# Performance work log

Measured on AMD Instinct MI355X. Metric: run time of the kernel, lower is better.

## Reference

```python
import jax, jax.numpy as jnp
import numpy as np

B, T, M, C, H = 2, 2048, 2048, 1024, 16
D = C // H  # head_size = 64


def setup_inputs() -> dict:
    key = jax.random.key(0)
    ks = jax.random.split(key, 8)
    s = 0.02
    return {
        "relative_positions": jax.random.normal(ks[0], (H, T, T + M), jnp.float32),
        "x": jax.random.normal(ks[1], (B, T, C), jnp.float32),
        "xl_memory": jax.random.normal(ks[2], (B, M, 2, C), jnp.float32),
        "Wq": jax.random.normal(ks[3], (C, C), jnp.float32) * s,
        "Wk": jax.random.normal(ks[4], (C, C), jnp.float32) * s,
        "Wv": jax.random.normal(ks[5], (C, C), jnp.float32) * s,
        "Wp": jax.random.normal(ks[6], (C, C), jnp.float32) * s,
        "bp": jax.random.normal(ks[7], (C,), jnp.float32) * s,
    }


def reference(relative_positions, x, xl_memory, Wq, Wk, Wv, Wp, bp):
    b, t, c = x.shape
    h, d = H, D
    q = x @ Wq  # [b,t,c]
    k = x @ Wk
    v = x @ Wv
    k_xl = xl_memory[..., 0, :]  # [b,m,c]
    v_xl = xl_memory[..., 1, :]
    k = jnp.concatenate([k_xl, k], axis=-2)  # [b,t+m,c]
    v = jnp.concatenate([v_xl, v], axis=-2)
    tk = k.shape[1]

    def split_heads(z):  # [b,s,(h d)] -> [b,h,s,d]
        return z.reshape(z.shape[0], z.shape[1], h, d).transpose(0, 2, 1, 3)

    qh, kh, vh = split_heads(q), split_heads(k), split_heads(v)
    w = jnp.einsum("bhid,bhjd->bhij", qh, kh)  # [b,h,t,tk]
    i, j = w.shape[-2], w.shape[-1]
    # bias added BEFORE scaling, as in the original
    w = (w + relative_positions[..., -i:, -j:]) * (d ** -0.5)
    # causal mask with memory offset: mask where col > row + (j - i)
    row = jnp.arange(i)[:, None]
    col = jnp.arange(j)[None, :]
    mask = col > row + (j - i)
    w = jnp.where(mask, -jnp.inf, w)
    w = jax.nn.softmax(w, axis=-1)
    wv = jnp.einsum("bhij,bhjd->bhid", w, vh)  # [b,h,t,d]
    wv = wv.transpose(0, 2, 1, 3).reshape(b, t, c)
    out = wv @ Wp + bp
    # rebuild xl memory from full-length k,v, keep last T steps
    k_flat = kh.transpose(0, 2, 1, 3).reshape(b, tk, c)
    v_flat = vh.transpose(0, 2, 1, 3).reshape(b, tk, c)
    new_xl_memory = jnp.stack([k_flat, v_flat], axis=-2)[:, -t:]  # [b,t,2,c]
    return out, new_xl_memory
```

## Files before the change

### kernel.cpp

```cpp
#include <hip/hip_runtime.h>
#include <hip/hip_bf16.h>

constexpr int NB  = 2;
constexpr int TT  = 2048;
constexpr int MEM = 2048;
constexpr int CC  = 1024;
constexpr int NH  = 16;
constexpr int HD  = 64;
constexpr int TKK = 4096;
constexpr int BT  = NB * TT;

typedef __attribute__((ext_vector_type(8))) short short8;
typedef __attribute__((ext_vector_type(4))) float floatx4;

struct __align__(8) us4 { unsigned short x, y, z, w; };

__device__ __forceinline__ unsigned short f2bf(float f) {
  union { float f; unsigned int u; } v; v.f = f;
  return (unsigned short)((v.u + 0x7fffu + ((v.u >> 16) & 1u)) >> 16);
}

__global__ __launch_bounds__(256) void prep_xl_k(const float* __restrict__ xl,
    unsigned short* __restrict__ k_ws, unsigned short* __restrict__ v_ws) {
  int idx = blockIdx.x * 256 + threadIdx.x;
  int c   = (idx & 255) << 2;
  int rem = idx >> 8;
  int m   = rem & 2047;
  int b   = rem >> 11;
  size_t src = ((size_t)(b * MEM + m)) * 2 * CC + c;
  float4 kk = *(const float4*)&xl[src];
  float4 vv = *(const float4*)&xl[src + CC];
  int h = c >> 6, d = c & 63;
  size_t dst = ((size_t)((b * NH + h) * TKK) + m) * HD + d;
  *(us4*)&k_ws[dst] = us4{f2bf(kk.x), f2bf(kk.y), f2bf(kk.z), f2bf(kk.w)};
  *(us4*)&v_ws[dst] = us4{f2bf(vv.x), f2bf(vv.y), f2bf(vv.z), f2bf(vv.w)};
}

__global__ __launch_bounds__(256) void gemm_qkv_k(
    const float* __restrict__ x, const float* __restrict__ Wq,
    const float* __restrict__ Wk, const float* __restrict__ Wv,
    unsigned short* __restrict__ q_ws, unsigned short* __restrict__ k_ws,
    unsigned short* __restrict__ v_ws, float* __restrict__ out_xl) {
  __shared__ unsigned short As[128][32];
  __shared__ unsigned short Bs[128][40];
  const int tid = threadIdx.x;
  const int m0 = blockIdx.x * 128;
  const int nb = blockIdx.y;
  const float* __restrict__ Wsrc = (nb < 8) ? Wq : ((nb < 16) ? Wk : Wv);
  const int n0 = (nb & 7) * 128;
  const int wave = tid >> 6, lane = tid & 63;
  const int mh = (wave >> 1) * 64, nh = (wave & 1) * 64;
  const int ln = lane & 15, qd = lane >> 4;
  const floatx4 fzero = {0.f, 0.f, 0.f, 0.f};

  floatx4 acc[4][4];
#pragma unroll
  for (int i = 0; i < 4; i++)
#pragma unroll
    for (int j = 0; j < 4; j++) acc[i][j] = fzero;

  for (int kt = 0; kt < CC; kt += 32) {
    __syncthreads();
#pragma unroll
    for (int i = 0; i < 4; i++) {
      int e = tid + i * 256;
      int row = e >> 3, kc = (e & 7) << 2;
      float4 a4 = *(const float4*)&x[(size_t)(m0 + row) * CC + kt + kc];
      *(us4*)&As[row][kc] = us4{f2bf(a4.x), f2bf(a4.y), f2bf(a4.z), f2bf(a4.w)};
    }
#pragma unroll
    for (int i = 0; i < 4; i++) {
      int e = tid + i * 256;
      int n = e & 127, kg = e >> 7;
      const float* p = &Wsrc[(size_t)(kt + kg * 4) * CC + n0 + n];
      float b0 = p[0], b1 = p[CC], b2 = p[2 * CC], b3 = p[3 * CC];
      *(us4*)&Bs[n][kg * 4] = us4{f2bf(b0), f2bf(b1), f2bf(b2), f2bf(b3)};
    }
    __syncthreads();
    short8 af[4], bfr[4];
#pragma unroll
    for (int mf = 0; mf < 4; mf++) af[mf]  = *(const short8*)&As[mh + mf * 16 + ln][qd * 8];
#pragma unroll
    for (int nf = 0; nf < 4; nf++) bfr[nf] = *(const short8*)&Bs[nh + nf * 16 + ln][qd * 8];
#pragma unroll
    for (int mf = 0; mf < 4; mf++)
#pragma unroll
      for (int nf = 0; nf < 4; nf++)
        acc[mf][nf] = __builtin_amdgcn_mfma_f32_16x16x32_bf16(af[mf], bfr[nf], acc[mf][nf], 0, 0, 0);
  }

  const int sel = nb >> 3;
#pragma unroll
  for (int mf = 0; mf < 4; mf++) {
#pragma unroll
    for (int nf = 0; nf < 4; nf++) {
      int gn = n0 + nh + nf * 16 + ln;
      int h = gn >> 6, d = gn & 63;
#pragma unroll
      for (int r = 0; r < 4; r++) {
        int gm = m0 + mh + mf * 16 + qd * 4 + r;
        int b = gm >> 11, t = gm & 2047;
        float val = acc[mf][nf][r];
        unsigned short bv = f2bf(val);
        if (sel == 0) {
          q_ws[((size_t)((b * NH + h) * TT) + t) * HD + d] = bv;
        } else if (sel == 1) {
          k_ws[((size_t)((b * NH + h) * TKK) + MEM + t) * HD + d] = bv;
          out_xl[(((size_t)(b * TT + t)) * 2 + 0) * CC + gn] = val;
        } else {
          v_ws[((size_t)((b * NH + h) * TKK) + MEM + t) * HD + d] = bv;
          out_xl[(((size_t)(b * TT + t)) * 2 + 1) * CC + gn] = val;
        }
      }
    }
  }
}

__global__ __launch_bounds__(256) void attn_k(
    const unsigned short* __restrict__ q_ws, const unsigned short* __restrict__ k_ws,
    const unsigned short* __restrict__ v_ws, const float* __restrict__ rel,
    unsigned short* __restrict__ wv_ws) {
  __shared__ unsigned short Ks[NB][64][72];
  __shared__ unsigned short Vs[NB][64][64];
  __shared__ unsigned short Ps[4][16][64];
  const int qt = blockIdx.x, h = blockIdx.y;
  const int tid = threadIdx.x;
  const int wave = tid >> 6, lane = tid & 63;
  const int ln = lane & 15, qd = lane >> 4;
  const int q0 = qt * 64;
  const int qrow_w = q0 + wave * 16;
  const floatx4 fzero = {0.f, 0.f, 0.f, 0.f};

  short8 qf[NB][2];
#pragma unroll
  for (int b = 0; b < NB; b++)
#pragma unroll
    for (int ks = 0; ks < 2; ks++)
      qf[b][ks] = *(const short8*)&q_ws[((size_t)((b * NH + h) * TT) + qrow_w + ln) * HD + ks * 32 + qd * 8];

  floatx4 of[NB][4];
  float mrow[NB][4], lrow[NB][4];
#pragma unroll
  for (int b = 0; b < NB; b++) {
#pragma unroll
    for (int nf = 0; nf < 4; nf++) of[b][nf] = fzero;
#pragma unroll
    for (int r = 0; r < 4; r++) { mrow[b][r] = -1e30f; lrow[b][r] = 0.f; }
  }

  const int ntiles = qt + 33;
  for (int kt = 0; kt < ntiles; kt++) {
    const int kbase = kt * 64;
    __syncthreads();
#pragma unroll
    for (int b = 0; b < NB; b++) {
      const size_t rowbase = (size_t)((b * NH + h) * TKK) + kbase;
#pragma unroll
      for (int i = 0; i < 2; i++) {
        int e = tid + i * 256;
        int r = e >> 3, c0 = (e & 7) << 3;
        *(short8*)&Ks[b][r][c0] = *(const short8*)&k_ws[(rowbase + r) * HD + c0];
        short8 v8 = *(const short8*)&v_ws[(rowbase + r) * HD + c0];
#pragma unroll
        for (int j = 0; j < 8; j++) {
          int d = c0 + j;
          int slot = ((r >> 3) ^ (d & 7) ^ (d >> 3)) & 7;
          Vs[b][d][(slot << 3) | (r & 7)] = (unsigned short)v8[j];
        }
      }
    }
    __syncthreads();

    float bias[4][4];
#pragma unroll
    for (int nf = 0; nf < 4; nf++)
#pragma unroll
      for (int r = 0; r < 4; r++)
        bias[nf][r] = rel[((size_t)(h * TT) + qrow_w + qd * 4 + r) * TKK + kbase + nf * 16 + ln];

    const bool lastTile = (kt == ntiles - 1);

#pragma unroll
    for (int b = 0; b < NB; b++) {
      floatx4 sacc[4];
#pragma unroll
      for (int nf = 0; nf < 4; nf++) sacc[nf] = fzero;
#pragma unroll
      for (int ks = 0; ks < 2; ks++)
#pragma unroll
        for (int nf = 0; nf < 4; nf++) {
          short8 kf = *(const short8*)&Ks[b][nf * 16 + ln][ks * 32 + qd * 8];
          sacc[nf] = __builtin_amdgcn_mfma_f32_16x16x32_bf16(qf[b][ks], kf, sacc[nf], 0, 0, 0);
        }

      float sv[4][4];
#pragma unroll
      for (int nf = 0; nf < 4; nf++)
#pragma unroll
        for (int r = 0; r < 4; r++)
          sv[nf][r] = (sacc[nf][r] + bias[nf][r]) * 0.125f;
      if (lastTile) {
#pragma unroll
        for (int nf = 0; nf < 4; nf++)
#pragma unroll
          for (int r = 0; r < 4; r++) {
            int kcol = kbase + nf * 16 + ln;
            int qrow = qrow_w + qd * 4 + r;
            if (kcol > qrow + MEM) sv[nf][r] = -1e30f;
          }
      }

#pragma unroll
      for (int r = 0; r < 4; r++) {
        float mx = fmaxf(fmaxf(sv[0][r], sv[1][r]), fmaxf(sv[2][r], sv[3][r]));
#pragma unroll
        for (int off = 8; off >= 1; off >>= 1)
          mx = fmaxf(mx, __shfl_xor(mx, off, 64));
        float mnew = fmaxf(mrow[b][r], mx);
        float alpha = __expf(mrow[b][r] - mnew);
        mrow[b][r] = mnew;
        float sum = 0.f;
#pragma unroll
        for (int nf = 0; nf < 4; nf++) {
          float p = __expf(sv[nf][r] - mnew);
          sv[nf][r] = p;
          sum += p;
        }
#pragma unroll
        for (int off = 8; off >= 1; off >>= 1)
          sum += __shfl_xor(sum, off, 64);
        lrow[b][r] = lrow[b][r] * alpha + sum;
#pragma unroll
        for (int nf = 0; nf < 4; nf++) of[b][nf][r] *= alpha;
      }

#pragma unroll
      for (int nf = 0; nf < 4; nf++)
#pragma unroll
        for (int r = 0; r < 4; r++) {
          int row = qd * 4 + r;
          int col = nf * 16 + ln;
          int slot = ((col >> 3) ^ (row & 7) ^ (row >> 3)) & 7;
          Ps[wave][row][(slot << 3) | (col & 7)] = f2bf(sv[nf][r]);
        }

#pragma unroll
      for (int ks = 0; ks < 2; ks++) {
        int g = qd + 4 * ks;
        int pslot = (g ^ (ln & 7) ^ (ln >> 3)) & 7;
        short8 pf = *(const short8*)&Ps[wave][ln][pslot << 3];
#pragma unroll
        for (int nf = 0; nf < 4; nf++) {
          int dd = nf * 16 + ln;
          int vslot = (g ^ (dd & 7) ^ (dd >> 3)) & 7;
          short8 vf = *(const short8*)&Vs[b][dd][vslot << 3];
          of[b][nf] = __builtin_amdgcn_mfma_f32_16x16x32_bf16(pf, vf, of[b][nf], 0, 0, 0);
        }
      }
    }
  }

#pragma unroll
  for (int b = 0; b < NB; b++) {
    float inv[4];
#pragma unroll
    for (int r = 0; r < 4; r++) inv[r] = 1.f / lrow[b][r];
#pragma unroll
    for (int nf = 0; nf < 4; nf++)
#pragma unroll
      for (int r = 0; r < 4; r++)
        wv_ws[((size_t)(b * TT) + qrow_w + qd * 4 + r) * CC + h * 64 + nf * 16 + ln] =
            f2bf(of[b][nf][r] * inv[r]);
  }
}

__global__ __launch_bounds__(256) void gemm_out_k(
    const unsigned short* __restrict__ a_bf, const float* __restrict__ Wp,
    const float* __restrict__ bp, float* __restrict__ out) {
  __shared__ unsigned short As[128][32];
  __shared__ unsigned short Bs[128][40];
  const int tid = threadIdx.x;
  const int m0 = blockIdx.x * 128;
  const int n0 = blockIdx.y * 128;
  const int wave = tid >> 6, lane = tid & 63;
  const int mh = (wave >> 1) * 64, nh = (wave & 1) * 64;
  const int ln = lane & 15, qd = lane >> 4;
  const floatx4 fzero = {0.f, 0.f, 0.f, 0.f};

  floatx4 acc[4][4];
#pragma unroll
  for (int i = 0; i < 4; i++)
#pragma unroll
    for (int j = 0; j < 4; j++) acc[i][j] = fzero;

  for (int kt = 0; kt < CC; kt += 32) {
    __syncthreads();
#pragma unroll
    for (int i = 0; i < 2; i++) {
      int e = tid + i * 256;
      int row = e >> 2, c0 = (e & 3) << 3;
      *(short8*)&As[row][c0] = *(const short8*)&a_bf[(size_t)(m0 + row) * CC + kt + c0];
    }
#pragma unroll
    for (int i = 0; i < 4; i++) {
      int e = tid + i * 256;
      int n = e & 127, kg = e >> 7;
      const float* p = &Wp[(size_t)(kt + kg * 4) * CC + n0 + n];
      float b0 = p[0], b1 = p[CC], b2 = p[2 * CC], b3 = p[3 * CC];
      *(us4*)&Bs[n][kg * 4] = us4{f2bf(b0), f2bf(b1), f2bf(b2), f2bf(b3)};
    }
    __syncthreads();
    short8 af[4], bfr[4];
#pragma unroll
    for (int mf = 0; mf < 4; mf++) af[mf]  = *(const short8*)&As[mh + mf * 16 + ln][qd * 8];
#pragma unroll
    for (int nf = 0; nf < 4; nf++) bfr[nf] = *(const short8*)&Bs[nh + nf * 16 + ln][qd * 8];
#pragma unroll
    for (int mf = 0; mf < 4; mf++)
#pragma unroll
      for (int nf = 0; nf < 4; nf++)
        acc[mf][nf] = __builtin_amdgcn_mfma_f32_16x16x32_bf16(af[mf], bfr[nf], acc[mf][nf], 0, 0, 0);
  }

#pragma unroll
  for (int mf = 0; mf < 4; mf++)
#pragma unroll
    for (int nf = 0; nf < 4; nf++) {
      int gn = n0 + nh + nf * 16 + ln;
      float bias = bp[gn];
#pragma unroll
      for (int r = 0; r < 4; r++) {
        int gm = m0 + mh + mf * 16 + qd * 4 + r;
        out[(size_t)gm * CC + gn] = acc[mf][nf][r] + bias;
      }
    }
}

extern "C" void kernel_launch(void* const* d_in, const int* in_sizes, int n_in,
                              void* d_out, int out_size, void* d_ws, size_t ws_size,
                              hipStream_t stream) {
  const float* rel = (const float*)d_in[0];
  const float* x   = (const float*)d_in[1];
  const float* xl  = (const float*)d_in[2];
  const float* Wq  = (const float*)d_in[3];
  const float* Wk  = (const float*)d_in[4];
  const float* Wv  = (const float*)d_in[5];
  const float* Wp  = (const float*)d_in[6];
  const float* bp  = (const float*)d_in[7];
  float* out    = (float*)d_out;
  float* out_xl = out + (size_t)BT * CC;

  char* ws = (char*)d_ws;
  unsigned short* q_ws  = (unsigned short*)(ws);
  unsigned short* k_ws  = (unsigned short*)(ws + (size_t)(8)  * 1024 * 1024);
  unsigned short* v_ws  = (unsigned short*)(ws + (size_t)(24) * 1024 * 1024);
  unsigned short* wv_ws = (unsigned short*)(ws + (size_t)(40) * 1024 * 1024);

  prep_xl_k<<<dim3(4096), dim3(256), 0, stream>>>(xl, k_ws, v_ws);
  gemm_qkv_k<<<dim3(32, 24), dim3(256), 0, stream>>>(x, Wq, Wk, Wv, q_ws, k_ws, v_ws, out_xl);
  attn_k<<<dim3(32, 16), dim3(256), 0, stream>>>(q_ws, k_ws, v_ws, rel, wv_ws);
  gemm_out_k<<<dim3(32, 8), dim3(256), 0, stream>>>(wv_ws, Wp, bp, out);
}
```

Before: 1.043 ms.

## Pre-transpose weights, pre-swizzle V, split attention per batch with register prefetch

Adds a kernel that converts Wq/Wk/Wv to bf16 and transposes them once, so the QKV GEMM loads B tiles with vector reads instead of strided scalar float reads. V is stored in a pre-swizzled transposed tile layout, so attention copies it straight into LDS without a per-element scatter. Attention now launches one block per (batch, query tile), which doubles the grid. It prefetches the next K/V tile into registers and computes the softmax denominator with an MFMA against a ones vector instead of shuffle reductions. The extra kernels and the Wt/wv_ws workspace aliasing (both at offset 40MB, used at different times) add launches and some risk, and the denominator is now summed from bf16-rounded probabilities.

```diff
diff --git a/kernel.cpp b/kernel.cpp
--- a/kernel.cpp
+++ b/kernel.cpp
@@ -19,35 +19,79 @@
   union { float f; unsigned int u; } v; v.f = f;
   return (unsigned short)((v.u + 0x7fffu + ((v.u >> 16) & 1u)) >> 16);
 }
+__device__ __forceinline__ unsigned short f2bf_fast(float f) {
+  union { float f; unsigned int u; } v; v.f = f;
+  return (unsigned short)((v.u + 0x8000u) >> 16);
+}
+
+__global__ __launch_bounds__(256) void prep_w_k(
+    const float* __restrict__ Wq, const float* __restrict__ Wk,
+    const float* __restrict__ Wv, unsigned short* __restrict__ Wt) {
+  __shared__ unsigned short T[64][72];
+  const int n0 = blockIdx.x * 64, k0 = blockIdx.y * 64, z = blockIdx.z;
+  const float* __restrict__ W = (z == 0) ? Wq : ((z == 1) ? Wk : Wv);
+  const int tid = threadIdx.x;
+#pragma unroll
+  for (int s = 0; s < 4; s++) {
+    int kr = (tid >> 4) + s * 16, nc = (tid & 15) << 2;
+    float4 w4 = *(const float4*)&W[(size_t)(k0 + kr) * CC + n0 + nc];
+    T[nc + 0][kr] = f2bf(w4.x);
+    T[nc + 1][kr] = f2bf(w4.y);
+    T[nc + 2][kr] = f2bf(w4.z);
+    T[nc + 3][kr] = f2bf(w4.w);
+  }
+  __syncthreads();
+#pragma unroll
+  for (int i = 0; i < 2; i++) {
+    int e = tid + i * 256;
+    int n = e >> 3, kc = (e & 7) << 3;
+    *(short8*)&Wt[(size_t)z * CC * CC + (size_t)(n0 + n) * CC + k0 + kc] =
+        *(const short8*)&T[n][kc];
+  }
+}
 
 __global__ __launch_bounds__(256) void prep_xl_k(const float* __restrict__ xl,
     unsigned short* __restrict__ k_ws, unsigned short* __restrict__ v_ws) {
-  int idx = blockIdx.x * 256 + threadIdx.x;
-  int c   = (idx & 255) << 2;
-  int rem = idx >> 8;
-  int m   = rem & 2047;
-  int b   = rem >> 11;
-  size_t src = ((size_t)(b * MEM + m)) * 2 * CC + c;
-  float4 kk = *(const float4*)&xl[src];
-  float4 vv = *(const float4*)&xl[src + CC];
-  int h = c >> 6, d = c & 63;
-  size_t dst = ((size_t)((b * NH + h) * TKK) + m) * HD + d;
-  *(us4*)&k_ws[dst] = us4{f2bf(kk.x), f2bf(kk.y), f2bf(kk.z), f2bf(kk.w)};
-  *(us4*)&v_ws[dst] = us4{f2bf(vv.x), f2bf(vv.y), f2bf(vv.z), f2bf(vv.w)};
+  __shared__ unsigned short T[64][72];
+  const int mt = blockIdx.x, h = blockIdx.y, b = blockIdx.z;
+  const int tid = threadIdx.x;
+  const int bh = b * NH + h;
+#pragma unroll
+  for (int s = 0; s < 4; s++) {
+    int m = (tid >> 4) + s * 16, d4 = (tid & 15) << 2;
+    size_t src = ((size_t)(b * MEM + mt * 64 + m)) * 2 * CC + h * 64 + d4;
+    float4 kk = *(const float4*)&xl[src];
+    float4 vv = *(const float4*)&xl[src + CC];
+    *(us4*)&k_ws[((size_t)bh * TKK + mt * 64 + m) * HD + d4] =
+        us4{f2bf(kk.x), f2bf(kk.y), f2bf(kk.z), f2bf(kk.w)};
+    T[d4 + 0][m] = f2bf(vv.x);
+    T[d4 + 1][m] = f2bf(vv.y);
+    T[d4 + 2][m] = f2bf(vv.z);
+    T[d4 + 3][m] = f2bf(vv.w);
+  }
+  __syncthreads();
+  const size_t vbase = ((size_t)bh * 64 + mt) * 4096;
+#pragma unroll
+  for (int i = 0; i < 2; i++) {
+    int e = tid + i * 256;
+    int d = e >> 3, mc = (e & 7) << 3;
+    int grp = (mc >> 3) ^ (d & 7);
+    *(short8*)&v_ws[vbase + d * 64 + (grp << 3)] = *(const short8*)&T[d][mc];
+  }
 }
 
 __global__ __launch_bounds__(256) void gemm_qkv_k(
-    const float* __restrict__ x, const float* __restrict__ Wq,
-    const float* __restrict__ Wk, const float* __restrict__ Wv,
+    const float* __restrict__ x, const unsigned short* __restrict__ Wt,
     unsigned short* __restrict__ q_ws, unsigned short* __restrict__ k_ws,
     unsigned short* __restrict__ v_ws, float* __restrict__ out_xl) {
-  __shared__ unsigned short As[128][32];
+  __shared__ unsigned short As[128][40];
   __shared__ unsigned short Bs[128][40];
   const int tid = threadIdx.x;
   const int m0 = blockIdx.x * 128;
   const int nb = blockIdx.y;
-  const float* __restrict__ Wsrc = (nb < 8) ? Wq : ((nb < 16) ? Wk : Wv);
+  const int sel = nb >> 3;
   const int n0 = (nb & 7) * 128;
+  const unsigned short* __restrict__ Wsel = Wt + (size_t)sel * CC * CC;
   const int wave = tid >> 6, lane = tid & 63;
   const int mh = (wave >> 1) * 64, nh = (wave & 1) * 64;
   const int ln = lane & 15, qd = lane >> 4;
@@ -69,12 +113,10 @@
       *(us4*)&As[row][kc] = us4{f2bf(a4.x), f2bf(a4.y), f2bf(a4.z), f2bf(a4.w)};
     }
 #pragma unroll
-    for (int i = 0; i < 4; i++) {
+    for (int i = 0; i < 2; i++) {
       int e = tid + i * 256;
-      int n = e & 127, kg = e >> 7;
-      const float* p = &Wsrc[(size_t)(kt + kg * 4) * CC + n0 + n];
-      float b0 = p[0], b1 = p[CC], b2 = p[2 * CC], b3 = p[3 * CC];
-      *(us4*)&Bs[n][kg * 4] = us4{f2bf(b0), f2bf(b1), f2bf(b2), f2bf(b3)};
+      int n = e >> 2, kc = (e & 3) << 3;
+      *(short8*)&Bs[n][kc] = *(const short8*)&Wsel[(size_t)(n0 + n) * CC + kt + kc];
     }
     __syncthreads();
     short8 af[4], bfr[4];
@@ -89,7 +131,6 @@
         acc[mf][nf] = __builtin_amdgcn_mfma_f32_16x16x32_bf16(af[mf], bfr[nf], acc[mf][nf], 0, 0, 0);
   }
 
-  const int sel = nb >> 3;
 #pragma unroll
   for (int mf = 0; mf < 4; mf++) {
 #pragma unroll
@@ -100,15 +141,19 @@
       for (int r = 0; r < 4; r++) {
         int gm = m0 + mh + mf * 16 + qd * 4 + r;
         int b = gm >> 11, t = gm & 2047;
+        int bh = b * NH + h;
         float val = acc[mf][nf][r];
         unsigned short bv = f2bf(val);
         if (sel == 0) {
-          q_ws[((size_t)((b * NH + h) * TT) + t) * HD + d] = bv;
+          q_ws[((size_t)bh * TT + t) * HD + d] = bv;
         } else if (sel == 1) {
-          k_ws[((size_t)((b * NH + h) * TKK) + MEM + t) * HD + d] = bv;
+          k_ws[((size_t)bh * TKK + MEM + t) * HD + d] = bv;
           out_xl[(((size_t)(b * TT + t)) * 2 + 0) * CC + gn] = val;
         } else {
-          v_ws[((size_t)((b * NH + h) * TKK) + MEM + t) * HD + d] = bv;
+          int kk = MEM + t;
+          int kblk = kk >> 6;
+          int grp = ((t >> 3) & 7) ^ (d & 7);
+          v_ws[((size_t)bh * 64 + kblk) * 4096 + d * 64 + (grp << 3) + (t & 7)] = bv;
           out_xl[(((size_t)(b * TT + t)) * 2 + 1) * CC + gn] = val;
         }
       }
@@ -116,168 +161,170 @@
   }
 }
 
-__global__ __launch_bounds__(256) void attn_k(
+__global__ __launch_bounds__(256, 4) void attn_k(
     const unsigned short* __restrict__ q_ws, const unsigned short* __restrict__ k_ws,
     const unsigned short* __restrict__ v_ws, const float* __restrict__ rel,
     unsigned short* __restrict__ wv_ws) {
-  __shared__ unsigned short Ks[NB][64][72];
-  __shared__ unsigned short Vs[NB][64][64];
+  __shared__ unsigned short Ks[64][72];
+  __shared__ unsigned short Vs[64 * 64];
   __shared__ unsigned short Ps[4][16][64];
-  const int qt = blockIdx.x, h = blockIdx.y;
+  const int bx = blockIdx.x;
+  const int b = bx & 1, qt = bx >> 1;
+  const int h = blockIdx.y;
   const int tid = threadIdx.x;
   const int wave = tid >> 6, lane = tid & 63;
   const int ln = lane & 15, qd = lane >> 4;
   const int q0 = qt * 64;
   const int qrow_w = q0 + wave * 16;
+  const int bh = b * NH + h;
   const floatx4 fzero = {0.f, 0.f, 0.f, 0.f};
 
-  short8 qf[NB][2];
-#pragma unroll
-  for (int b = 0; b < NB; b++)
-#pragma unroll
-    for (int ks = 0; ks < 2; ks++)
-      qf[b][ks] = *(const short8*)&q_ws[((size_t)((b * NH + h) * TT) + qrow_w + ln) * HD + ks * 32 + qd * 8];
-
-  floatx4 of[NB][4];
-  float mrow[NB][4], lrow[NB][4];
-#pragma unroll
-  for (int b = 0; b < NB; b++) {
-#pragma unroll
-    for (int nf = 0; nf < 4; nf++) of[b][nf] = fzero;
-#pragma unroll
-    for (int r = 0; r < 4; r++) { mrow[b][r] = -1e30f; lrow[b][r] = 0.f; }
-  }
+  const unsigned short* __restrict__ kbaseP = k_ws + (size_t)bh * TKK * HD;
+  const unsigned short* __restrict__ vbaseP = v_ws + (size_t)bh * 64 * 4096;
+  const float* __restrict__ relBase = rel + ((size_t)h * TT + qrow_w + qd * 4) * TKK + ln;
+
+  short8 qf[2];
+#pragma unroll
+  for (int ks = 0; ks < 2; ks++)
+    qf[ks] = *(const short8*)&q_ws[((size_t)bh * TT + qrow_w + ln) * HD + ks * 32 + qd * 8];
+
+  short8 ones;
+#pragma unroll
+  for (int j = 0; j < 8; j++) ones[j] = (short)0x3F80;
+
+  floatx4 of[4], osum = fzero;
+  float mrow[4];
+#pragma unroll
+  for (int nf = 0; nf < 4; nf++) of[nf] = fzero;
+#pragma unroll
+  for (int r = 0; r < 4; r++) mrow[r] = -1e30f;
 
   const int ntiles = qt + 33;
+  short8 kpre0, kpre1, vpre0, vpre1;
+  {
+    const unsigned short* kp = kbaseP;
+    const unsigned short* vp = vbaseP;
+    kpre0 = *(const short8*)(kp + tid * 8);
+    kpre1 = *(const short8*)(kp + tid * 8 + 2048);
+    vpre0 = *(const short8*)(vp + tid * 8);
+    vpre1 = *(const short8*)(vp + tid * 8 + 2048);
+  }
+
   for (int kt = 0; kt < ntiles; kt++) {
     const int kbase = kt * 64;
     __syncthreads();
-#pragma unroll
-    for (int b = 0; b < NB; b++) {
-      const size_t rowbase = (size_t)((b * NH + h) * TKK) + kbase;
-#pragma unroll
-      for (int i = 0; i < 2; i++) {
-        int e = tid + i * 256;
-        int r = e >> 3, c0 = (e & 7) << 3;
-        *(short8*)&Ks[b][r][c0] = *(const short8*)&k_ws[(rowbase + r) * HD + c0];
-        short8 v8 = *(const short8*)&v_ws[(rowbase + r) * HD + c0];
-#pragma unroll
-        for (int j = 0; j < 8; j++) {
-          int d = c0 + j;
-          int slot = ((r >> 3) ^ (d & 7) ^ (d >> 3)) & 7;
-          Vs[b][d][(slot << 3) | (r & 7)] = (unsigned short)v8[j];
+    {
+      int r0 = tid >> 3, c0 = (tid & 7) << 3;
+      *(short8*)&Ks[r0][c0] = kpre0;
+      *(short8*)&Ks[r0 + 32][c0] = kpre1;
+      *(short8*)&Vs[tid * 8] = vpre0;
+      *(short8*)&Vs[tid * 8 + 2048] = vpre1;
+    }
+    __syncthreads();
+    if (kt + 1 < ntiles) {
+      const unsigned short* kp = kbaseP + (kt + 1) * 4096;
+      const unsigned short* vp = vbaseP + (kt + 1) * 4096;
+      kpre0 = *(const short8*)(kp + tid * 8);
+      kpre1 = *(const short8*)(kp + tid * 8 + 2048);
+      vpre0 = *(const short8*)(vp + tid * 8);
+      vpre1 = *(const short8*)(vp + tid * 8 + 2048);
+    }
+
+    float bias[4][4];
+#pragma unroll
+    for (int nf = 0; nf < 4; nf++)
+#pragma unroll
+      for (int r = 0; r < 4; r++)
+        bias[nf][r] = relBase[(size_t)r * TKK + kbase + nf * 16];
+
+    floatx4 sacc[4];
+#pragma unroll
+    for (int nf = 0; nf < 4; nf++) sacc[nf] = fzero;
+#pragma unroll
+    for (int ks = 0; ks < 2; ks++)
+#pragma unroll
+      for (int nf = 0; nf < 4; nf++) {
+        short8 kf = *(const short8*)&Ks[nf * 16 + ln][ks * 32 + qd * 8];
+        sacc[nf] = __builtin_amdgcn_mfma_f32_16x16x32_bf16(qf[ks], kf, sacc[nf], 0, 0, 0);
+      }
+
+    float sv[4][4];
+#pragma unroll
+    for (int nf = 0; nf < 4; nf++)
+#pragma unroll
+      for (int r = 0; r < 4; r++)
+        sv[nf][r] = (sacc[nf][r] + bias[nf][r]) * 0.125f;
+
+    if (kt == ntiles - 1) {
+#pragma unroll
+      for (int nf = 0; nf < 4; nf++)
+#pragma unroll
+        for (int r = 0; r < 4; r++) {
+          int kcol = kbase + nf * 16 + ln;
+          int qrow = qrow_w + qd * 4 + r;
+          if (kcol > qrow + MEM) sv[nf][r] = -1e30f;
         }
-      }
-    }
-    __syncthreads();
-
-    float bias[4][4];
+    }
+
+#pragma unroll
+    for (int r = 0; r < 4; r++) {
+      float mx = fmaxf(fmaxf(sv[0][r], sv[1][r]), fmaxf(sv[2][r], sv[3][r]));
+#pragma unroll
+      for (int off = 8; off >= 1; off >>= 1)
+        mx = fmaxf(mx, __shfl_xor(mx, off, 64));
+      float mnew = fmaxf(mrow[r], mx);
+      float alpha = __expf(mrow[r] - mnew);
+      mrow[r] = mnew;
+#pragma unroll
+      for (int nf = 0; nf < 4; nf++) {
+        float p = __expf(sv[nf][r] - mnew);
+        sv[nf][r] = p;
+        of[nf][r] *= alpha;
+      }
+      osum[r] *= alpha;
+    }
+
 #pragma unroll
     for (int nf = 0; nf < 4; nf++)
 #pragma unroll
-      for (int r = 0; r < 4; r++)
-        bias[nf][r] = rel[((size_t)(h * TT) + qrow_w + qd * 4 + r) * TKK + kbase + nf * 16 + ln];
-
-    const bool lastTile = (kt == ntiles - 1);
-
-#pragma unroll
-    for (int b = 0; b < NB; b++) {
-      floatx4 sacc[4];
-#pragma unroll
-      for (int nf = 0; nf < 4; nf++) sacc[nf] = fzero;
-#pragma unroll
-      for (int ks = 0; ks < 2; ks++)
-#pragma unroll
-        for (int nf = 0; nf < 4; nf++) {
-          short8 kf = *(const short8*)&Ks[b][nf * 16 + ln][ks * 32 + qd * 8];
-          sacc[nf] = __builtin_amdgcn_mfma_f32_16x16x32_bf16(qf[b][ks], kf, sacc[nf], 0, 0, 0);
-        }
-
-      float sv[4][4];
-#pragma unroll
-      for (int nf = 0; nf < 4; nf++)
-#pragma unroll
-        for (int r = 0; r < 4; r++)
-          sv[nf][r] = (sacc[nf][r] + bias[nf][r]) * 0.125f;
-      if (lastTile) {
-#pragma unroll
-        for (int nf = 0; nf < 4; nf++)
-#pragma unroll
-          for (int r = 0; r < 4; r++) {
-            int kcol = kbase + nf * 16 + ln;
-            int qrow = qrow_w + qd * 4 + r;
-            if (kcol > qrow + MEM) sv[nf][r] = -1e30f;
-          }
-      }
-
-#pragma unroll
       for (int r = 0; r < 4; r++) {
-        float mx = fmaxf(fmaxf(sv[0][r], sv[1][r]), fmaxf(sv[2][r], sv[3][r]));
-#pragma unroll
-        for (int off = 8; off >= 1; off >>= 1)
-          mx = fmaxf(mx, __shfl_xor(mx, off, 64));
-        float mnew = fmaxf(mrow[b][r], mx);
-        float alpha = __expf(mrow[b][r] - mnew);
-        mrow[b][r] = mnew;
-        float sum = 0.f;
-#pragma unroll
-        for (int nf = 0; nf < 4; nf++) {
-          float p = __expf(sv[nf][r] - mnew);
-          sv[nf][r] = p;
-          sum += p;
-        }
-#pragma unroll
-        for (int off = 8; off >= 1; off >>= 1)
-          sum += __shfl_xor(sum, off, 64);
-        lrow[b][r] = lrow[b][r] * alpha + sum;
-#pragma unroll
-        for (int nf = 0; nf < 4; nf++) of[b][nf][r] *= alpha;
-      }
-
-#pragma unroll
-      for (int nf = 0; nf < 4; nf++)
-#pragma unroll
-        for (int r = 0; r < 4; r++) {
-          int row = qd * 4 + r;
-          int col = nf * 16 + ln;
-          int slot = ((col >> 3) ^ (row & 7) ^ (row >> 3)) & 7;
-          Ps[wave][row][(slot << 3) | (col & 7)] = f2bf(sv[nf][r]);
-        }
-
-#pragma unroll
-      for (int ks = 0; ks < 2; ks++) {
-        int g = qd + 4 * ks;
-        int pslot = (g ^ (ln & 7) ^ (ln >> 3)) & 7;
-        short8 pf = *(const short8*)&Ps[wave][ln][pslot << 3];
-#pragma unroll
-        for (int nf = 0; nf < 4; nf++) {
-          int dd = nf * 16 + ln;
-          int vslot = (g ^ (dd & 7) ^ (dd >> 3)) & 7;
-          short8 vf = *(const short8*)&Vs[b][dd][vslot << 3];
-          of[b][nf] = __builtin_amdgcn_mfma_f32_16x16x32_bf16(pf, vf, of[b][nf], 0, 0, 0);
-        }
-      }
-    }
-  }
-
-#pragma unroll
-  for (int b = 0; b < NB; b++) {
-    float inv[4];
-#pragma unroll
-    for (int r = 0; r < 4; r++) inv[r] = 1.f / lrow[b][r];
-#pragma unroll
-    for (int nf = 0; nf < 4; nf++)
-#pragma unroll
-      for (int r = 0; r < 4; r++)
-        wv_ws[((size_t)(b * TT) + qrow_w + qd * 4 + r) * CC + h * 64 + nf * 16 + ln] =
-            f2bf(of[b][nf][r] * inv[r]);
-  }
+        int row = qd * 4 + r;
+        int col = nf * 16 + ln;
+        int slot = ((col >> 3) ^ (row & 7) ^ (row >> 3)) & 7;
+        Ps[wave][row][(slot << 3) | (col & 7)] = f2bf_fast(sv[nf][r]);
+      }
+
+#pragma unroll
+    for (int ks = 0; ks < 2; ks++) {
+      int g = ks * 4 + qd;
+      int pslot = (g ^ (ln & 7) ^ (ln >> 3)) & 7;
+      short8 pf = *(const short8*)&Ps[wave][ln][pslot << 3];
+      osum = __builtin_amdgcn_mfma_f32_16x16x32_bf16(pf, ones, osum, 0, 0, 0);
+#pragma unroll
+      for (int nf = 0; nf < 4; nf++) {
+        int dd = nf * 16 + ln;
+        int vgrp = g ^ (dd & 7);
+        short8 vf = *(const short8*)&Vs[dd * 64 + (vgrp << 3)];
+        of[nf] = __builtin_amdgcn_mfma_f32_16x16x32_bf16(pf, vf, of[nf], 0, 0, 0);
+      }
+    }
+  }
+
+  float inv[4];
+#pragma unroll
+  for (int r = 0; r < 4; r++) inv[r] = 1.f / osum[r];
+#pragma unroll
+  for (int nf = 0; nf < 4; nf++)
+#pragma unroll
+    for (int r = 0; r < 4; r++)
+      wv_ws[((size_t)(b * TT) + qrow_w + qd * 4 + r) * CC + h * 64 + nf * 16 + ln] =
+          f2bf(of[nf][r] * inv[r]);
 }
 
 __global__ __launch_bounds__(256) void gemm_out_k(
     const unsigned short* __restrict__ a_bf, const float* __restrict__ Wp,
     const float* __restrict__ bp, float* __restrict__ out) {
-  __shared__ unsigned short As[128][32];
+  __shared__ unsigned short As[128][40];
   __shared__ unsigned short Bs[128][40];
   const int tid = threadIdx.x;
   const int m0 = blockIdx.x * 128;
@@ -352,12 +399,14 @@
 
   char* ws = (char*)d_ws;
   unsigned short* q_ws  = (unsigned short*)(ws);
-  unsigned short* k_ws  = (unsigned short*)(ws + (size_t)(8)  * 1024 * 1024);
-  unsigned short* v_ws  = (unsigned short*)(ws + (size_t)(24) * 1024 * 1024);
-  unsigned short* wv_ws = (unsigned short*)(ws + (size_t)(40) * 1024 * 1024);
-
-  prep_xl_k<<<dim3(4096), dim3(256), 0, stream>>>(xl, k_ws, v_ws);
-  gemm_qkv_k<<<dim3(32, 24), dim3(256), 0, stream>>>(x, Wq, Wk, Wv, q_ws, k_ws, v_ws, out_xl);
-  attn_k<<<dim3(32, 16), dim3(256), 0, stream>>>(q_ws, k_ws, v_ws, rel, wv_ws);
+  unsigned short* k_ws  = (unsigned short*)(ws + (size_t)8  * 1024 * 1024);
+  unsigned short* v_ws  = (unsigned short*)(ws + (size_t)24 * 1024 * 1024);
+  unsigned short* Wt    = (unsigned short*)(ws + (size_t)40 * 1024 * 1024);
+  unsigned short* wv_ws = (unsigned short*)(ws + (size_t)40 * 1024 * 1024);
+
+  prep_w_k<<<dim3(16, 16, 3), dim3(256), 0, stream>>>(Wq, Wk, Wv, Wt);
+  prep_xl_k<<<dim3(32, 16, 2), dim3(256), 0, stream>>>(xl, k_ws, v_ws);
+  gemm_qkv_k<<<dim3(32, 24), dim3(256), 0, stream>>>(x, Wt, q_ws, k_ws, v_ws, out_xl);
+  attn_k<<<dim3(64, 16), dim3(256), 0, stream>>>(q_ws, k_ws, v_ws, rel, wv_ws);
   gemm_out_k<<<dim3(32, 8), dim3(256), 0, stream>>>(wv_ws, Wp, bp, out);
 }
```

New measurement: 1.093 ms. 1.05x slower.
